# Kernel optimization log

Measured on AMD Instinct MI355X. Metric: run time of the kernel, lower is better.

## Reference

```python
import jax, jax.numpy as jnp
import numpy as np
import math

B, D, C = 256, 512, 100000
SCALE = 64.0
MARGIN = 0.5
ALPHA = 1.2
SIGMA = 2.0
THRESH = math.cos(math.pi - MARGIN)
MM = math.sin(math.pi - MARGIN) * MARGIN


def _l2_normalize(x, axis=-1, eps=1e-12):
    n = jnp.linalg.norm(x, axis=axis, keepdims=True)
    return x / jnp.maximum(n, eps)


def setup_inputs() -> dict:
    key = jax.random.key(0)
    k1, k2, k3 = jax.random.split(key, 3)
    inp = jax.random.normal(k1, (B, D), dtype=jnp.float32)
    label = jax.random.randint(k2, (B,), 0, C, dtype=jnp.int64)
    stdv = 1.0 / math.sqrt(D)
    weight = jax.random.uniform(k3, (C, D), dtype=jnp.float32, minval=-stdv, maxval=stdv)
    return {"input": inp, "label": label, "weight": weight}


def reference(input, label, weight):
    # cosine similarity: [B, C]
    cos = _l2_normalize(input) @ _l2_normalize(weight).T
    rows = jnp.arange(cos.shape[0])
    cos_lb = cos[rows, label]  # [B]
    # angular margin on the target logit, with the standard arcface fallback
    a_lb = jnp.where(
        cos_lb > THRESH,
        jnp.cos(jnp.arccos(jnp.clip(cos_lb, -1.0, 1.0)) + MARGIN),
        cos_lb - MM,
    )  # [B]
    # gaussian reweighting of negatives around the margined target logit (detached)
    t_scale = jax.lax.stop_gradient(
        ALPHA * jnp.exp(-jnp.square(cos - a_lb[:, None]) / SIGMA)
    )  # [B, C]
    onehot = jax.nn.one_hot(label, cos.shape[1], dtype=cos.dtype)  # [B, C]
    logits = SCALE * (
        onehot * a_lb[:, None] + (1.0 - onehot) * (t_scale * cos + t_scale - 1.0)
    )
    return logits
```

## Files before the change

kernel.cpp:

```cpp
#include <hip/hip_runtime.h>
#include <hip/hip_bf16.h>
#include <math.h>

#define B_ 256
#define D_ 512
#define C_ 100000

#define SCALE_  64.0f
#define ALPHA_  1.2f
#define THRESH_ (-0.8775825618903728f)
#define MM_     (0.23971276930210156f)
#define COSM_   (0.8775825618903728f)
#define SINM_   (0.4794255386042030f)

typedef __bf16 bf16x8 __attribute__((ext_vector_type(8)));
typedef __bf16 bf16x4 __attribute__((ext_vector_type(4)));
typedef float  f32x4  __attribute__((ext_vector_type(4)));

__global__ void prep_kernel(const float* __restrict__ inp,
                            const int* __restrict__ lab_raw,
                            const float* __restrict__ weight,
                            __bf16* __restrict__ xnf,
                            float* __restrict__ a_lb,
                            int* __restrict__ lab32) {
    const int b = blockIdx.x;
    const int l = threadIdx.x;

    const bool is64 = (lab_raw[1] == 0) & (lab_raw[3] == 0) & (lab_raw[5] == 0) &
                      (lab_raw[7] == 0) & (lab_raw[9] == 0) & (lab_raw[11] == 0) &
                      (lab_raw[13] == 0) & (lab_raw[15] == 0);
    const int lab = is64 ? lab_raw[2 * b] : lab_raw[b];

    const float* ip = inp + b * D_ + l * 8;
    f32x4 v0 = *(const f32x4*)ip;
    f32x4 v1 = *(const f32x4*)(ip + 4);
    float ss = v0.x * v0.x + v0.y * v0.y + v0.z * v0.z + v0.w * v0.w +
               v1.x * v1.x + v1.y * v1.y + v1.z * v1.z + v1.w * v1.w;
#pragma unroll
    for (int m = 1; m < 64; m <<= 1) ss += __shfl_xor(ss, m);
    const float ninv = 1.0f / fmaxf(sqrtf(ss), 1e-12f);

    float xf[8] = {v0.x * ninv, v0.y * ninv, v0.z * ninv, v0.w * ninv,
                   v1.x * ninv, v1.y * ninv, v1.z * ninv, v1.w * ninv};
    bf16x8 xv;
#pragma unroll
    for (int i = 0; i < 8; ++i) xv[i] = (__bf16)xf[i];

    const int tile_idx = (b >> 4) * 16 + (l >> 2);
    const int lf = (b & 15) + ((l & 3) << 4);
    *(bf16x8*)((char*)xnf + tile_idx * 1024 + lf * 16) = xv;

    const float* wp = weight + (size_t)lab * D_ + l * 8;
    f32x4 w0 = *(const f32x4*)wp;
    f32x4 w1 = *(const f32x4*)(wp + 4);
    float wss = w0.x * w0.x + w0.y * w0.y + w0.z * w0.z + w0.w * w0.w +
                w1.x * w1.x + w1.y * w1.y + w1.z * w1.z + w1.w * w1.w;
    float dp = xf[0] * w0.x + xf[1] * w0.y + xf[2] * w0.z + xf[3] * w0.w +
               xf[4] * w1.x + xf[5] * w1.y + xf[6] * w1.z + xf[7] * w1.w;
#pragma unroll
    for (int m = 1; m < 64; m <<= 1) {
        wss += __shfl_xor(wss, m);
        dp  += __shfl_xor(dp, m);
    }
    if (l == 0) {
        const float cos_lb = dp / fmaxf(sqrtf(wss), 1e-12f);
        const float ccl = fminf(fmaxf(cos_lb, -1.0f), 1.0f);
        const float s = sqrtf(fmaxf(0.0f, 1.0f - ccl * ccl));
        const float a1 = ccl * COSM_ - s * SINM_;
        a_lb[b] = (cos_lb > THRESH_) ? a1 : (cos_lb - MM_);
        lab32[b] = lab;
    }
}

#define BN 32

__global__ __launch_bounds__(256, 3)
void gemm_kernel(const __bf16* __restrict__ xnf,
                 const float* __restrict__ weight,
                 const float* __restrict__ a_lb,
                 const int* __restrict__ lab32,
                 float* __restrict__ out) {
    __shared__ __align__(16) char wT[BN * D_ * 2];
    __shared__ float wssq[BN];

    const int tid  = threadIdx.x;
    const int lane = tid & 63;
    const int w    = tid >> 6;
    const int n0   = blockIdx.x * BN;

    f32x4 acc[4][2] = {};

    const float* wpanel = weight + (size_t)(n0 + w * 8) * D_;

    f32x4 wva[8], wvb[8];
#pragma unroll
    for (int i = 0; i < 8; ++i)
        wva[i] = *(const f32x4*)(wpanel + (i >> 1) * D_ + (i & 1) * 256 + lane * 4);
#pragma unroll
    for (int i = 0; i < 8; ++i)
        wvb[i] = *(const f32x4*)(wpanel + ((i + 8) >> 1) * D_ + (i & 1) * 256 + lane * 4);

    bf16x8 af[2][4];
#pragma unroll
    for (int m = 0; m < 4; ++m)
        af[0][m] = *(const bf16x8*)((const char*)xnf + ((w * 4 + m) * 16 + 0) * 1024 + lane * 16);

#pragma unroll
    for (int c = 0; c < 2; ++c) {
        float ss = 0.0f;
#pragma unroll
        for (int i = 0; i < 8; ++i) {
            f32x4 v = (c == 0) ? wva[i] : wvb[i];
            ss += v.x * v.x + v.y * v.y + v.z * v.z + v.w * v.w;
            bf16x4 h;
            h[0] = (__bf16)v.x; h[1] = (__bf16)v.y;
            h[2] = (__bf16)v.z; h[3] = (__bf16)v.w;
            const int row = w * 8 + c * 4 + (i >> 1);
            int off = row * (D_ * 2) + (i & 1) * 512 + lane * 8;
            off ^= (row & 7) << 4;
            *(bf16x4*)(wT + off) = h;
            if (i & 1) {
#pragma unroll
                for (int msk = 1; msk < 64; msk <<= 1) ss += __shfl_xor(ss, msk);
                if (lane == 0) wssq[row] = ss;
                ss = 0.0f;
            }
        }
    }
    __syncthreads();

    bf16x8 bfr[2][2];
#pragma unroll
    for (int n = 0; n < 2; ++n) {
        const int row = n * 16 + (lane & 15);
        int off = row * (D_ * 2) + 0 * 64 + (lane >> 4) * 16;
        off ^= (row & 7) << 4;
        bfr[0][n] = *(const bf16x8*)(wT + off);
    }

    for (int ks = 0; ks < 16; ++ks) {
        const int cur = ks & 1, nxt = cur ^ 1;
        if (ks < 15) {
#pragma unroll
            for (int m = 0; m < 4; ++m)
                af[nxt][m] = *(const bf16x8*)((const char*)xnf +
                             ((w * 4 + m) * 16 + ks + 1) * 1024 + lane * 16);
#pragma unroll
            for (int n = 0; n < 2; ++n) {
                const int row = n * 16 + (lane & 15);
                int off = row * (D_ * 2) + (ks + 1) * 64 + (lane >> 4) * 16;
                off ^= (row & 7) << 4;
                bfr[nxt][n] = *(const bf16x8*)(wT + off);
            }
        }
#pragma unroll
        for (int m = 0; m < 4; ++m)
#pragma unroll
            for (int n = 0; n < 2; ++n)
                acc[m][n] = __builtin_amdgcn_mfma_f32_16x16x32_bf16(
                    af[cur][m], bfr[cur][n], acc[m][n], 0, 0, 0);
    }

    float al_r[16];
    int   lb_r[16];
    const int rb0 = w * 64 + ((lane >> 4) << 2);
#pragma unroll
    for (int m = 0; m < 4; ++m)
#pragma unroll
        for (int j = 0; j < 4; ++j) {
            const int b = rb0 + m * 16 + j;
            al_r[m * 4 + j] = a_lb[b];
            lb_r[m * 4 + j] = lab32[b];
        }

#pragma unroll
    for (int n = 0; n < 2; ++n) {
        const int ln = n * 16 + (lane & 15);
        const int c = n0 + ln;
        const float winv = 1.0f / fmaxf(sqrtf(wssq[ln]), 1e-12f);
#pragma unroll
        for (int m = 0; m < 4; ++m)
#pragma unroll
            for (int j = 0; j < 4; ++j) {
                const int b = rb0 + m * 16 + j;
                const float al = al_r[m * 4 + j];
                const float cosv = acc[m][n][j] * winv;
                const float d = cosv - al;
                const float t = ALPHA_ * __expf(-0.5f * d * d);
                const float o = (c == lb_r[m * 4 + j]) ? al : (t * cosv + t - 1.0f);
                out[(size_t)b * C_ + c] = SCALE_ * o;
            }
    }
}

extern "C" void kernel_launch(void* const* d_in, const int* in_sizes, int n_in,
                              void* d_out, int out_size, void* d_ws, size_t ws_size,
                              hipStream_t stream) {
    const float* inp = (const float*)d_in[0];
    const int*   lab = (const int*)d_in[1];
    const float* w   = (const float*)d_in[2];
    float* out = (float*)d_out;

    char* ws = (char*)d_ws;
    __bf16* xnf  = (__bf16*)ws;
    float*  a_lb = (float*)(ws + 262144);
    int*    l32  = (int*)(ws + 262144 + 1024);

    prep_kernel<<<B_, 64, 0, stream>>>(inp, lab, w, xnf, a_lb, l32);
    gemm_kernel<<<C_ / BN, 256, 0, stream>>>(xnf, w, a_lb, l32, out);
}
```

Before: 89.59 us.

## Make GEMM persistent with register-resident A and double-buffered weight panels

Replaces the one-block-per-panel launch with a persistent grid of 256 blocks of 512 threads. Each block loops over weight panels with a stride of the grid size and double-buffers the bf16 panel in LDS. Each wave keeps its full 32-row slice of normalized input in registers for the whole run, so xnf is no longer re-read from global memory for every panel. The next panel's global loads are prefetched into registers while the current panel computes, overlapping weight fetch with MFMA and the output stores. The cost is higher register pressure and a block-wide barrier per panel.

```diff
diff --git a/kernel.cpp b/kernel.cpp
--- a/kernel.cpp
+++ b/kernel.cpp
@@ -5,6 +5,9 @@
 #define B_ 256
 #define D_ 512
 #define C_ 100000
+#define BN 32
+#define NBLK 256
+#define NPAN (C_ / BN)
 
 #define SCALE_  64.0f
 #define ALPHA_  1.2f
@@ -72,124 +75,143 @@
     }
 }
 
-#define BN 32
-
-__global__ __launch_bounds__(256, 3)
+__device__ __forceinline__ void stage_panel(const f32x4* wv, char* wbuf,
+                                            float* wsq, int w, int lane) {
+    float ss = 0.0f;
+#pragma unroll
+    for (int i = 0; i < 8; ++i) {
+        f32x4 v = wv[i];
+        ss += v.x * v.x + v.y * v.y + v.z * v.z + v.w * v.w;
+        bf16x4 h;
+        h[0] = (__bf16)v.x; h[1] = (__bf16)v.y;
+        h[2] = (__bf16)v.z; h[3] = (__bf16)v.w;
+        const int row = w * 4 + (i >> 1);
+        int off = (row << 10) + ((i & 1) << 9) + lane * 8;
+        off ^= (row & 7) << 4;
+        *(bf16x4*)(wbuf + off) = h;
+        if (i & 1) {
+#pragma unroll
+            for (int msk = 1; msk < 64; msk <<= 1) ss += __shfl_xor(ss, msk);
+            if (lane == 0) wsq[row] = ss;
+            ss = 0.0f;
+        }
+    }
+}
+
+__global__ __launch_bounds__(512, 2)
 void gemm_kernel(const __bf16* __restrict__ xnf,
                  const float* __restrict__ weight,
                  const float* __restrict__ a_lb,
                  const int* __restrict__ lab32,
                  float* __restrict__ out) {
-    __shared__ __align__(16) char wT[BN * D_ * 2];
-    __shared__ float wssq[BN];
+    __shared__ __align__(16) char wT[2][BN * D_ * 2];
+    __shared__ float wssq[2][BN];
 
     const int tid  = threadIdx.x;
     const int lane = tid & 63;
     const int w    = tid >> 6;
-    const int n0   = blockIdx.x * BN;
-
-    f32x4 acc[4][2] = {};
-
-    const float* wpanel = weight + (size_t)(n0 + w * 8) * D_;
-
-    f32x4 wva[8], wvb[8];
-#pragma unroll
-    for (int i = 0; i < 8; ++i)
-        wva[i] = *(const f32x4*)(wpanel + (i >> 1) * D_ + (i & 1) * 256 + lane * 4);
-#pragma unroll
-    for (int i = 0; i < 8; ++i)
-        wvb[i] = *(const f32x4*)(wpanel + ((i + 8) >> 1) * D_ + (i & 1) * 256 + lane * 4);
-
-    bf16x8 af[2][4];
-#pragma unroll
-    for (int m = 0; m < 4; ++m)
-        af[0][m] = *(const bf16x8*)((const char*)xnf + ((w * 4 + m) * 16 + 0) * 1024 + lane * 16);
-
-#pragma unroll
-    for (int c = 0; c < 2; ++c) {
-        float ss = 0.0f;
-#pragma unroll
-        for (int i = 0; i < 8; ++i) {
-            f32x4 v = (c == 0) ? wva[i] : wvb[i];
-            ss += v.x * v.x + v.y * v.y + v.z * v.z + v.w * v.w;
-            bf16x4 h;
-            h[0] = (__bf16)v.x; h[1] = (__bf16)v.y;
-            h[2] = (__bf16)v.z; h[3] = (__bf16)v.w;
-            const int row = w * 8 + c * 4 + (i >> 1);
-            int off = row * (D_ * 2) + (i & 1) * 512 + lane * 8;
+    const int bid  = blockIdx.x;
+    const int npan = (NPAN - bid + NBLK - 1) / NBLK;
+
+    f32x4 wv[8];
+    {
+        const float* wp = weight + (size_t)(bid * BN + w * 4) * D_;
+#pragma unroll
+        for (int i = 0; i < 8; ++i)
+            wv[i] = *(const f32x4*)(wp + (i >> 1) * D_ + (i & 1) * 256 + lane * 4);
+    }
+
+    bf16x8 af[2][16];
+#pragma unroll
+    for (int m = 0; m < 2; ++m)
+#pragma unroll
+        for (int kt = 0; kt < 16; ++kt)
+            af[m][kt] = *(const bf16x8*)((const char*)xnf +
+                          (((2 * w + m) * 16 + kt) << 10) + lane * 16);
+
+    float al_r[8];
+    int   lb_r[8];
+    const int rb0 = w * 32 + ((lane >> 4) << 2);
+#pragma unroll
+    for (int m = 0; m < 2; ++m)
+#pragma unroll
+        for (int j = 0; j < 4; ++j) {
+            al_r[m * 4 + j] = a_lb[rb0 + m * 16 + j];
+            lb_r[m * 4 + j] = lab32[rb0 + m * 16 + j];
+        }
+
+    stage_panel(wv, wT[0], wssq[0], w, lane);
+    if (npan > 1) {
+        const float* wp = weight + (size_t)((bid + NBLK) * BN + w * 4) * D_;
+#pragma unroll
+        for (int i = 0; i < 8; ++i)
+            wv[i] = *(const f32x4*)(wp + (i >> 1) * D_ + (i & 1) * 256 + lane * 4);
+    }
+    __syncthreads();
+
+    for (int it = 0; it < npan; ++it) {
+        const int n0 = (bid + it * NBLK) * BN;
+        const char* wb = wT[it & 1];
+
+        f32x4 acc[2][2] = {};
+        bf16x8 bfr[2][2];
+#pragma unroll
+        for (int n = 0; n < 2; ++n) {
+            const int row = n * 16 + (lane & 15);
+            int off = (row << 10) + ((lane >> 4) << 4);
             off ^= (row & 7) << 4;
-            *(bf16x4*)(wT + off) = h;
-            if (i & 1) {
-#pragma unroll
-                for (int msk = 1; msk < 64; msk <<= 1) ss += __shfl_xor(ss, msk);
-                if (lane == 0) wssq[row] = ss;
-                ss = 0.0f;
+            bfr[0][n] = *(const bf16x8*)(wb + off);
+        }
+#pragma unroll
+        for (int kt = 0; kt < 16; ++kt) {
+            const int cb = kt & 1;
+            if (kt < 15) {
+#pragma unroll
+                for (int n = 0; n < 2; ++n) {
+                    const int row = n * 16 + (lane & 15);
+                    int off = (row << 10) + ((kt + 1) << 6) + ((lane >> 4) << 4);
+                    off ^= (row & 7) << 4;
+                    bfr[cb ^ 1][n] = *(const bf16x8*)(wb + off);
+                }
             }
-        }
-    }
-    __syncthreads();
-
-    bf16x8 bfr[2][2];
-#pragma unroll
-    for (int n = 0; n < 2; ++n) {
-        const int row = n * 16 + (lane & 15);
-        int off = row * (D_ * 2) + 0 * 64 + (lane >> 4) * 16;
-        off ^= (row & 7) << 4;
-        bfr[0][n] = *(const bf16x8*)(wT + off);
-    }
-
-    for (int ks = 0; ks < 16; ++ks) {
-        const int cur = ks & 1, nxt = cur ^ 1;
-        if (ks < 15) {
-#pragma unroll
-            for (int m = 0; m < 4; ++m)
-                af[nxt][m] = *(const bf16x8*)((const char*)xnf +
-                             ((w * 4 + m) * 16 + ks + 1) * 1024 + lane * 16);
-#pragma unroll
-            for (int n = 0; n < 2; ++n) {
-                const int row = n * 16 + (lane & 15);
-                int off = row * (D_ * 2) + (ks + 1) * 64 + (lane >> 4) * 16;
-                off ^= (row & 7) << 4;
-                bfr[nxt][n] = *(const bf16x8*)(wT + off);
+#pragma unroll
+            for (int m = 0; m < 2; ++m)
+#pragma unroll
+                for (int n = 0; n < 2; ++n)
+                    acc[m][n] = __builtin_amdgcn_mfma_f32_16x16x32_bf16(
+                        af[m][kt], bfr[cb][n], acc[m][n], 0, 0, 0);
+        }
+
+#pragma unroll
+        for (int n = 0; n < 2; ++n) {
+            const int ln = n * 16 + (lane & 15);
+            const int c = n0 + ln;
+            const float winv = 1.0f / fmaxf(sqrtf(wssq[it & 1][ln]), 1e-12f);
+#pragma unroll
+            for (int m = 0; m < 2; ++m)
+#pragma unroll
+                for (int j = 0; j < 4; ++j) {
+                    const float al = al_r[m * 4 + j];
+                    const float cosv = acc[m][n][j] * winv;
+                    const float d = cosv - al;
+                    const float t = ALPHA_ * __expf(-0.5f * d * d);
+                    const float o = (c == lb_r[m * 4 + j]) ? al
+                                                           : (t * cosv + t - 1.0f);
+                    out[(size_t)(rb0 + m * 16 + j) * C_ + c] = SCALE_ * o;
+                }
+        }
+
+        if (it + 1 < npan) {
+            stage_panel(wv, wT[(it + 1) & 1], wssq[(it + 1) & 1], w, lane);
+            if (it + 2 < npan) {
+                const float* wp = weight +
+                    (size_t)((bid + (it + 2) * NBLK) * BN + w * 4) * D_;
+#pragma unroll
+                for (int i = 0; i < 8; ++i)
+                    wv[i] = *(const f32x4*)(wp + (i >> 1) * D_ + (i & 1) * 256 + lane * 4);
             }
         }
-#pragma unroll
-        for (int m = 0; m < 4; ++m)
-#pragma unroll
-            for (int n = 0; n < 2; ++n)
-                acc[m][n] = __builtin_amdgcn_mfma_f32_16x16x32_bf16(
-                    af[cur][m], bfr[cur][n], acc[m][n], 0, 0, 0);
-    }
-
-    float al_r[16];
-    int   lb_r[16];
-    const int rb0 = w * 64 + ((lane >> 4) << 2);
-#pragma unroll
-    for (int m = 0; m < 4; ++m)
-#pragma unroll
-        for (int j = 0; j < 4; ++j) {
-            const int b = rb0 + m * 16 + j;
-            al_r[m * 4 + j] = a_lb[b];
-            lb_r[m * 4 + j] = lab32[b];
-        }
-
-#pragma unroll
-    for (int n = 0; n < 2; ++n) {
-        const int ln = n * 16 + (lane & 15);
-        const int c = n0 + ln;
-        const float winv = 1.0f / fmaxf(sqrtf(wssq[ln]), 1e-12f);
-#pragma unroll
-        for (int m = 0; m < 4; ++m)
-#pragma unroll
-            for (int j = 0; j < 4; ++j) {
-                const int b = rb0 + m * 16 + j;
-                const float al = al_r[m * 4 + j];
-                const float cosv = acc[m][n][j] * winv;
-                const float d = cosv - al;
-                const float t = ALPHA_ * __expf(-0.5f * d * d);
-                const float o = (c == lb_r[m * 4 + j]) ? al : (t * cosv + t - 1.0f);
-                out[(size_t)b * C_ + c] = SCALE_ * o;
-            }
+        __syncthreads();
     }
 }
 
@@ -207,5 +229,5 @@
     int*    l32  = (int*)(ws + 262144 + 1024);
 
     prep_kernel<<<B_, 64, 0, stream>>>(inp, lab, w, xnf, a_lb, l32);
-    gemm_kernel<<<C_ / BN, 256, 0, stream>>>(xnf, w, a_lb, l32, out);
-}
+    gemm_kernel<<<NBLK, 512, 0, stream>>>(xnf, w, a_lb, l32, out);
+}
```

Result: slower. 117.3 us (+30.9%).

## Load weight fragments directly from global into MFMA registers, dropping LDS staging

Applied to the files above, without the earlier changes.

The GEMM kernel no longer stages the bf16-converted weight panel in shared memory behind a barrier. Each wave now reads fp32 weights straight into B-fragment layout, converts them to bf16 in registers, and accumulates row sums of squares per lane, reduced with two shuffles. This removes the LDS writes and reads, the swizzle math and the __syncthreads. In exchange, all four waves redundantly fetch the same weight panel from global memory with a strided per-row access pattern, so the design relies on L1/L2 hits.

```diff
diff --git a/kernel.cpp b/kernel.cpp
--- a/kernel.cpp
+++ b/kernel.cpp
@@ -5,6 +5,7 @@
 #define B_ 256
 #define D_ 512
 #define C_ 100000
+#define BN 32
 
 #define SCALE_  64.0f
 #define ALPHA_  1.2f
@@ -14,7 +15,6 @@
 #define SINM_   (0.4794255386042030f)
 
 typedef __bf16 bf16x8 __attribute__((ext_vector_type(8)));
-typedef __bf16 bf16x4 __attribute__((ext_vector_type(4)));
 typedef float  f32x4  __attribute__((ext_vector_type(4)));
 
 __global__ void prep_kernel(const float* __restrict__ inp,
@@ -72,123 +72,93 @@
     }
 }
 
-#define BN 32
-
 __global__ __launch_bounds__(256, 3)
 void gemm_kernel(const __bf16* __restrict__ xnf,
                  const float* __restrict__ weight,
                  const float* __restrict__ a_lb,
                  const int* __restrict__ lab32,
                  float* __restrict__ out) {
-    __shared__ __align__(16) char wT[BN * D_ * 2];
-    __shared__ float wssq[BN];
-
     const int tid  = threadIdx.x;
     const int lane = tid & 63;
     const int w    = tid >> 6;
     const int n0   = blockIdx.x * BN;
+    const int lr   = lane & 15;
+    const int lk   = lane >> 4;
 
     f32x4 acc[4][2] = {};
+    float ssq[2] = {0.0f, 0.0f};
 
-    const float* wpanel = weight + (size_t)(n0 + w * 8) * D_;
-
-    f32x4 wva[8], wvb[8];
-#pragma unroll
-    for (int i = 0; i < 8; ++i)
-        wva[i] = *(const f32x4*)(wpanel + (i >> 1) * D_ + (i & 1) * 256 + lane * 4);
-#pragma unroll
-    for (int i = 0; i < 8; ++i)
-        wvb[i] = *(const f32x4*)(wpanel + ((i + 8) >> 1) * D_ + (i & 1) * 256 + lane * 4);
-
-    bf16x8 af[2][4];
-#pragma unroll
-    for (int m = 0; m < 4; ++m)
-        af[0][m] = *(const bf16x8*)((const char*)xnf + ((w * 4 + m) * 16 + 0) * 1024 + lane * 16);
+    const float* wb = weight + (size_t)(n0 + lr) * D_ + lk * 8;
+    const char*  ab = (const char*)xnf + (size_t)(w * 4 * 16) * 1024 + lane * 16;
 
 #pragma unroll
-    for (int c = 0; c < 2; ++c) {
-        float ss = 0.0f;
+    for (int kt = 0; kt < 8; ++kt) {
+        bf16x8 bw[2][2];
 #pragma unroll
-        for (int i = 0; i < 8; ++i) {
-            f32x4 v = (c == 0) ? wva[i] : wvb[i];
-            ss += v.x * v.x + v.y * v.y + v.z * v.z + v.w * v.w;
-            bf16x4 h;
-            h[0] = (__bf16)v.x; h[1] = (__bf16)v.y;
-            h[2] = (__bf16)v.z; h[3] = (__bf16)v.w;
-            const int row = w * 8 + c * 4 + (i >> 1);
-            int off = row * (D_ * 2) + (i & 1) * 512 + lane * 8;
-            off ^= (row & 7) << 4;
-            *(bf16x4*)(wT + off) = h;
-            if (i & 1) {
+        for (int n = 0; n < 2; ++n) {
 #pragma unroll
-                for (int msk = 1; msk < 64; msk <<= 1) ss += __shfl_xor(ss, msk);
-                if (lane == 0) wssq[row] = ss;
-                ss = 0.0f;
+            for (int ks = 0; ks < 2; ++ks) {
+                const float* p = wb + (size_t)n * 16 * D_ + kt * 64 + ks * 32;
+                f32x4 lo = *(const f32x4*)(p);
+                f32x4 hi = *(const f32x4*)(p + 4);
+                ssq[n] += lo.x * lo.x + lo.y * lo.y + lo.z * lo.z + lo.w * lo.w +
+                          hi.x * hi.x + hi.y * hi.y + hi.z * hi.z + hi.w * hi.w;
+                bf16x8 h;
+                h[0] = (__bf16)lo.x; h[1] = (__bf16)lo.y;
+                h[2] = (__bf16)lo.z; h[3] = (__bf16)lo.w;
+                h[4] = (__bf16)hi.x; h[5] = (__bf16)hi.y;
+                h[6] = (__bf16)hi.z; h[7] = (__bf16)hi.w;
+                bw[ks][n] = h;
             }
         }
-    }
-    __syncthreads();
-
-    bf16x8 bfr[2][2];
-#pragma unroll
-    for (int n = 0; n < 2; ++n) {
-        const int row = n * 16 + (lane & 15);
-        int off = row * (D_ * 2) + 0 * 64 + (lane >> 4) * 16;
-        off ^= (row & 7) << 4;
-        bfr[0][n] = *(const bf16x8*)(wT + off);
-    }
-
-    for (int ks = 0; ks < 16; ++ks) {
-        const int cur = ks & 1, nxt = cur ^ 1;
-        if (ks < 15) {
-#pragma unroll
-            for (int m = 0; m < 4; ++m)
-                af[nxt][m] = *(const bf16x8*)((const char*)xnf +
-                             ((w * 4 + m) * 16 + ks + 1) * 1024 + lane * 16);
-#pragma unroll
-            for (int n = 0; n < 2; ++n) {
-                const int row = n * 16 + (lane & 15);
-                int off = row * (D_ * 2) + (ks + 1) * 64 + (lane >> 4) * 16;
-                off ^= (row & 7) << 4;
-                bfr[nxt][n] = *(const bf16x8*)(wT + off);
-            }
-        }
+        bf16x8 af[2][4];
 #pragma unroll
         for (int m = 0; m < 4; ++m)
 #pragma unroll
-            for (int n = 0; n < 2; ++n)
-                acc[m][n] = __builtin_amdgcn_mfma_f32_16x16x32_bf16(
-                    af[cur][m], bfr[cur][n], acc[m][n], 0, 0, 0);
+            for (int ks = 0; ks < 2; ++ks)
+                af[ks][m] = *(const bf16x8*)(ab + ((size_t)m * 16 + kt * 2 + ks) * 1024);
+
+#pragma unroll
+        for (int ks = 0; ks < 2; ++ks)
+#pragma unroll
+            for (int m = 0; m < 4; ++m)
+#pragma unroll
+                for (int n = 0; n < 2; ++n)
+                    acc[m][n] = __builtin_amdgcn_mfma_f32_16x16x32_bf16(
+                        af[ks][m], bw[ks][n], acc[m][n], 0, 0, 0);
+    }
+
+#pragma unroll
+    for (int n = 0; n < 2; ++n) {
+        ssq[n] += __shfl_xor(ssq[n], 16);
+        ssq[n] += __shfl_xor(ssq[n], 32);
     }
 
     float al_r[16];
     int   lb_r[16];
-    const int rb0 = w * 64 + ((lane >> 4) << 2);
+    const int rb0 = w * 64 + (lk << 2);
 #pragma unroll
     for (int m = 0; m < 4; ++m)
 #pragma unroll
         for (int j = 0; j < 4; ++j) {
-            const int b = rb0 + m * 16 + j;
-            al_r[m * 4 + j] = a_lb[b];
-            lb_r[m * 4 + j] = lab32[b];
+            al_r[m * 4 + j] = a_lb[rb0 + m * 16 + j];
+            lb_r[m * 4 + j] = lab32[rb0 + m * 16 + j];
         }
 
 #pragma unroll
     for (int n = 0; n < 2; ++n) {
-        const int ln = n * 16 + (lane & 15);
-        const int c = n0 + ln;
-        const float winv = 1.0f / fmaxf(sqrtf(wssq[ln]), 1e-12f);
+        const int c = n0 + n * 16 + lr;
+        const float winv = 1.0f / fmaxf(sqrtf(ssq[n]), 1e-12f);
 #pragma unroll
         for (int m = 0; m < 4; ++m)
 #pragma unroll
             for (int j = 0; j < 4; ++j) {
-                const int b = rb0 + m * 16 + j;
                 const float al = al_r[m * 4 + j];
                 const float cosv = acc[m][n][j] * winv;
                 const float d = cosv - al;
                 const float t = ALPHA_ * __expf(-0.5f * d * d);
                 const float o = (c == lb_r[m * 4 + j]) ? al : (t * cosv + t - 1.0f);
-                out[(size_t)b * C_ + c] = SCALE_ * o;
+                out[(size_t)(rb0 + m * 16 + j) * C_ + c] = SCALE_ * o;
             }
     }
 }
```

Measured after the change: 168.6 us. +88.2%, slower.
